# Kernel optimization log

Hardware: AMD Instinct MI355X
Metric: run time of the kernel (lower is better)

Reference implementation:

```python
import jax, jax.numpy as jnp
import numpy as np
from jax import lax

WINDOW_SIZE = 11
CHANNEL = 3
SIGMA = 1.5


def _build_window():
    # 1D gaussian, normalized, then outer product -> (C, 1, k, k) depthwise kernel
    coords = jnp.arange(WINDOW_SIZE, dtype=jnp.float32) - WINDOW_SIZE // 2
    g = jnp.exp(-coords ** 2 / (2.0 * SIGMA ** 2))
    g = g / g.sum()
    w2d = jnp.outer(g, g)  # (k, k)
    return jnp.broadcast_to(w2d[None, None], (CHANNEL, 1, WINDOW_SIZE, WINDOW_SIZE))


def _dwconv(x, w):
    pad = WINDOW_SIZE // 2
    return lax.conv_general_dilated(
        x, w,
        window_strides=(1, 1),
        padding=[(pad, pad), (pad, pad)],
        dimension_numbers=("NCHW", "OIHW", "NCHW"),
        feature_group_count=CHANNEL,
    )


def setup_inputs() -> dict:
    key = jax.random.key(0)
    k1, k2 = jax.random.split(key)
    pred = jax.random.uniform(k1, (16, 3, 512, 512), dtype=jnp.float32)
    target = jax.random.uniform(k2, (16, 3, 512, 512), dtype=jnp.float32)
    return {"pred": pred, "target": target}


def reference(pred, target):
    C1, C2 = 0.01 ** 2, 0.03 ** 2
    w = _build_window().astype(pred.dtype)

    mu_x = _dwconv(pred, w)
    mu_y = _dwconv(target, w)
    mu_x_sq = mu_x * mu_x
    mu_y_sq = mu_y * mu_y
    mu_xy = mu_x * mu_y

    sg_x = _dwconv(pred * pred, w) - mu_x_sq
    sg_y = _dwconv(target * target, w) - mu_y_sq
    sg_xy = _dwconv(pred * target, w) - mu_xy

    ssim_map = ((2.0 * mu_xy + C1) * (2.0 * sg_xy + C2)) / (
        (mu_x_sq + mu_y_sq + C1) * (sg_x + sg_y + C2)
    )
    return 1.0 - ssim_map.mean()
```

## Files before the change

kernel.cpp:

```cpp
#include <hip/hip_runtime.h>


namespace {
constexpr int IMG   = 512;
constexpr int NCH   = 48;
constexpr int TW    = 16;
constexpr int TH    = 64;
constexpr int RSTR  = 88;
constexpr int NSTR  = (TH + 16) / 16;
constexpr int TPX   = IMG / TW;
constexpr int TPY   = IMG / TH;
constexpr int NBLK  = TPX * TPY * NCH;

constexpr float Wf[11] = {
    0.00102838f, 0.00759876f, 0.03600077f, 0.10936069f, 0.21300554f,
    0.26601172f,
    0.21300554f, 0.10936069f, 0.03600077f, 0.00759876f, 0.00102838f };

constexpr float band_wc(int d) {
    return (d >= 0 && d < 11) ? Wf[d] : 0.f;
}

constexpr unsigned short f2h(float f) {
    if (f == 0.f) return 0;
    unsigned u = __builtin_bit_cast(unsigned, f);
    int  he = int((u >> 23) & 0xff) - 127 + 15;
    unsigned hm   = (u & 0x7fffff) >> 13;
    unsigned rest = u & 0x1fff;
    if (rest > 0x1000 || (rest == 0x1000 && (hm & 1))) ++hm;
    return (unsigned short)((unsigned(he) << 10) + hm);
}

struct Tabs { unsigned short a[64][8]; unsigned short b[64][8]; };
constexpr Tabs build_tabs() {
    Tabs t{};
    for (int lane = 0; lane < 64; ++lane) {
        const int nr = lane & 15, quad = lane >> 4;
        for (int jj = 0; jj < 8; ++jj) {
            const int k = quad * 8 + jj;
            t.a[lane][jj] = f2h(band_wc(k - nr));
            t.b[lane][jj] = f2h(band_wc(k - nr - 3));
        }
    }
    return t;
}
}

__device__ __constant__ __align__(16) Tabs g_tabs = build_tabs();

typedef _Float16 half8 __attribute__((ext_vector_type(8)));
typedef _Float16 half4v __attribute__((ext_vector_type(4)));
typedef _Float16 h2 __attribute__((ext_vector_type(2)));
typedef float float4v __attribute__((ext_vector_type(4)));
typedef float float2v __attribute__((ext_vector_type(2)));

__device__ inline h2 pk(float a, float b) {
    auto v = __builtin_amdgcn_cvt_pkrtz(a, b);
    h2 r;
    __builtin_memcpy(&r, &v, sizeof(r));
    return r;
}

union H8 { half8 v; h2 p[4]; };

__global__ __launch_bounds__(256, 8) void ssim_tile_kernel(
    const float* __restrict__ pred, const float* __restrict__ tgt,
    float* __restrict__ partial)
{
    __shared__ __align__(16) _Float16 hf_t[5][TW][RSTR];
    __shared__ float wred[4];

    const int t    = threadIdx.x;
    const int w    = t >> 6;
    const int lane = t & 63;
    const int nr   = lane & 15;
    const int quad = lane >> 4;

    const int bid  = blockIdx.x;
    const int img  = bid >> 8;
    const int tile = bid & 255;
    const int txi  = tile >> 3;
    const int tyi  = tile & 7;
    const int tx   = txi * TW;
    const int ty   = tyi * TH;

    const float* __restrict__ p = pred + (size_t)img * (IMG * IMG);
    const float* __restrict__ q = tgt  + (size_t)img * (IMG * IMG);

    const half8 Aband = *(const half8*)(g_tabs.a[lane]);
    const half8 Bband = *(const half8*)(g_tabs.b[lane]);
    const float4v zf = {0.f, 0.f, 0.f, 0.f};
    const half8 z8 = {};

    const int cb  = tx - 8 + (quad << 3);
    const int cbc = min(max(cb, 0), IMG - 8);
    const bool okc = ((unsigned)cb <= (unsigned)(IMG - 8));

    auto ld_stripe = [&](int s, float4& xa, float4& xb, float4& ya, float4& yb) {
        const int gy  = ty + 16 * s + nr - 5;
        const int gyc = min(max(gy, 0), IMG - 1);
        const float* rp = p + gyc * IMG + cbc;
        const float* rq = q + gyc * IMG + cbc;
        xa = *(const float4*)rp;
        xb = *(const float4*)(rp + 4);
        ya = *(const float4*)rq;
        yb = *(const float4*)(rq + 4);
    };

    auto proc_stripe = [&](int s, float4 xa, float4 xb, float4 ya, float4 yb) {
        const int gy = ty + 16 * s + nr - 5;
        const bool ok = ((unsigned)gy < (unsigned)IMG) && okc;

        H8 ax, ay;
        ax.p[0] = pk(xa.x, xa.y); ax.p[1] = pk(xa.z, xa.w);
        ax.p[2] = pk(xb.x, xb.y); ax.p[3] = pk(xb.z, xb.w);
        ay.p[0] = pk(ya.x, ya.y); ay.p[1] = pk(ya.z, ya.w);
        ay.p[2] = pk(yb.x, yb.y); ay.p[3] = pk(yb.z, yb.w);
        if (!ok) { ax.v = z8; ay.v = z8; }

        half8 fx  = ax.v;
        half8 fy  = ay.v;
        half8 fxx = fx * fx;
        half8 fyy = fy * fy;
        half8 fxy = fx * fy;

        float4v D[5];
        D[0] = __builtin_amdgcn_mfma_f32_16x16x32_f16(fx,  Bband, zf, 0, 0, 0);
        D[1] = __builtin_amdgcn_mfma_f32_16x16x32_f16(fy,  Bband, zf, 0, 0, 0);
        D[2] = __builtin_amdgcn_mfma_f32_16x16x32_f16(fxx, Bband, zf, 0, 0, 0);
        D[3] = __builtin_amdgcn_mfma_f32_16x16x32_f16(fyy, Bband, zf, 0, 0, 0);
        D[4] = __builtin_amdgcn_mfma_f32_16x16x32_f16(fxy, Bband, zf, 0, 0, 0);

        const int r0 = 16 * s + (quad << 2);
        #pragma unroll
        for (int f = 0; f < 5; ++f) {
            h2 lo = pk(D[f][0], D[f][1]);
            h2 hi = pk(D[f][2], D[f][3]);
            half4v hh = {lo[0], lo[1], hi[0], hi[1]};
            *(half4v*)&hf_t[f][nr][r0] = hh;
        }
    };

    {
        float4 xa0, xb0, ya0, yb0;
        ld_stripe(w, xa0, xb0, ya0, yb0);
        if (w == 0) {
            float4 xa1, xb1, ya1, yb1;
            ld_stripe(4, xa1, xb1, ya1, yb1);
            proc_stripe(0, xa0, xb0, ya0, yb0);
            proc_stripe(4, xa1, xb1, ya1, yb1);
        } else {
            proc_stripe(w, xa0, xb0, ya0, yb0);
        }
    }
    __syncthreads();

    constexpr float C1 = 1e-4f, C2 = 9e-4f;
    const float2v C1v = {C1, C1};
    const float2v C2v = {C2, C2};
    const float2v K12 = {C1 + C2, C1 + C2};
    float2v lsum2 = {0.f, 0.f};
    {
        const int rb = 16 * w + (quad << 3);
        float4v acc[5];
        #pragma unroll
        for (int f = 0; f < 5; ++f) {
            half8 bf = *(const half8*)&hf_t[f][nr][rb];
            acc[f] = __builtin_amdgcn_mfma_f32_16x16x32_f16(Aband, bf, zf, 0, 0, 0);
        }
        #pragma unroll
        for (int h = 0; h < 2; ++h) {
            float2v mx  = {acc[0][2*h], acc[0][2*h+1]};
            float2v my  = {acc[1][2*h], acc[1][2*h+1]};
            float2v ex2 = {acc[2][2*h], acc[2][2*h+1]};
            float2v ey2 = {acc[3][2*h], acc[3][2*h+1]};
            float2v exy = {acc[4][2*h], acc[4][2*h+1]};
            float2v P  = mx * my;
            float2v U  = mx * mx + my * my + C1v;
            float2v n1 = 2.f * P + C1v;
            float2v n2 = 2.f * (exy - P) + C2v;
            float2v num = n1 * n2;
            float2v e1 = (ex2 + ey2) - U + K12;
            float2v den = U * e1;
            float2v r = {__builtin_amdgcn_rcpf(den.x),
                         __builtin_amdgcn_rcpf(den.y)};
            lsum2 += num * r;
        }
    }
    float lsum = lsum2.x + lsum2.y;

    #pragma unroll
    for (int off = 32; off > 0; off >>= 1)
        lsum += __shfl_down(lsum, off, 64);
    if (lane == 0) wred[w] = lsum;
    __syncthreads();
    if (t == 0) partial[bid] = wred[0] + wred[1] + wred[2] + wred[3];
}

__global__ __launch_bounds__(1024) void ssim_finish(
    const float* __restrict__ partial, float* __restrict__ out)
{
    __shared__ float wred[16];
    const int t = threadIdx.x;
    float s = 0.f;
    #pragma unroll
    for (int i = 0; i < NBLK / 1024; ++i)
        s += partial[t + i * 1024];
    #pragma unroll
    for (int off = 32; off > 0; off >>= 1)
        s += __shfl_down(s, off, 64);
    if ((t & 63) == 0) wred[t >> 6] = s;
    __syncthreads();
    if (t == 0) {
        float acc = 0.f;
        #pragma unroll
        for (int i = 0; i < 16; ++i) acc += wred[i];
        out[0] = 1.f - acc * (1.f / (float)((long long)NCH * IMG * IMG));
    }
}

extern "C" void kernel_launch(void* const* d_in, const int* in_sizes, int n_in,
                              void* d_out, int out_size, void* d_ws, size_t ws_size,
                              hipStream_t stream)
{
    const float* pred = (const float*)d_in[0];
    const float* tgt  = (const float*)d_in[1];
    float* out     = (float*)d_out;
    float* partial = (float*)d_ws;

    ssim_tile_kernel<<<NBLK, 256, 0, stream>>>(pred, tgt, partial);
    ssim_finish<<<1, 1024, 0, stream>>>(partial, out);
}
```

Measured before the change: 139.1 us.

## Give each wave an independent 16x16 tile and drop block-level barriers

Restructures the SSIM kernel so each wavefront computes a full 16x16 output tile on its own, loading its 32-row halo and doing both horizontal and vertical band MFMAs through a per-wave LDS slot. This removes __syncthreads and the uneven stripe split in which one wave handled two stripes. In exchange, input halo reads and horizontal MFMA work per output double, and per-tile partial sums grow fourfold for the finish kernel. LDS use per field is reduced by reusing two slots sequentially.

```diff
diff --git a/kernel.cpp b/kernel.cpp
--- a/kernel.cpp
+++ b/kernel.cpp
@@ -4,13 +4,10 @@
 namespace {
 constexpr int IMG   = 512;
 constexpr int NCH   = 48;
-constexpr int TW    = 16;
-constexpr int TH    = 64;
-constexpr int RSTR  = 88;
-constexpr int NSTR  = (TH + 16) / 16;
-constexpr int TPX   = IMG / TW;
-constexpr int TPY   = IMG / TH;
-constexpr int NBLK  = TPX * TPY * NCH;
+constexpr int TPX   = IMG / 16;
+constexpr int NTILE = TPX * TPX * NCH;
+constexpr int NBLK  = NTILE / 4;
+constexpr int RS    = 40;
 
 constexpr float Wf[11] = {
     0.00102838f, 0.00759876f, 0.03600077f, 0.10936069f, 0.21300554f,
@@ -63,12 +60,11 @@
 
 union H8 { half8 v; h2 p[4]; };
 
-__global__ __launch_bounds__(256, 8) void ssim_tile_kernel(
+__global__ __launch_bounds__(256, 6) void ssim_fused_kernel(
     const float* __restrict__ pred, const float* __restrict__ tgt,
     float* __restrict__ partial)
 {
-    __shared__ __align__(16) _Float16 hf_t[5][TW][RSTR];
-    __shared__ float wred[4];
+    __shared__ __align__(16) _Float16 hf[4][2][16][RS];
 
     const int t    = threadIdx.x;
     const int w    = t >> 6;
@@ -76,13 +72,11 @@
     const int nr   = lane & 15;
     const int quad = lane >> 4;
 
-    const int bid  = blockIdx.x;
-    const int img  = bid >> 8;
-    const int tile = bid & 255;
-    const int txi  = tile >> 3;
-    const int tyi  = tile & 7;
-    const int tx   = txi * TW;
-    const int ty   = tyi * TH;
+    const int tid  = blockIdx.x * 4 + w;
+    const int img  = tid >> 10;
+    const int tile = tid & 1023;
+    const int tx   = (tile & 31) * 16;
+    const int ty   = (tile >> 5) * 16;
 
     const float* __restrict__ p = pred + (size_t)img * (IMG * IMG);
     const float* __restrict__ q = tgt  + (size_t)img * (IMG * IMG);
@@ -96,105 +90,92 @@
     const int cbc = min(max(cb, 0), IMG - 8);
     const bool okc = ((unsigned)cb <= (unsigned)(IMG - 8));
 
-    auto ld_stripe = [&](int s, float4& xa, float4& xb, float4& ya, float4& yb) {
+    float4 xa[2], xb[2], ya[2], yb[2];
+    bool ok[2];
+    #pragma unroll
+    for (int s = 0; s < 2; ++s) {
         const int gy  = ty + 16 * s + nr - 5;
         const int gyc = min(max(gy, 0), IMG - 1);
+        ok[s] = ((unsigned)gy < (unsigned)IMG) && okc;
         const float* rp = p + gyc * IMG + cbc;
         const float* rq = q + gyc * IMG + cbc;
-        xa = *(const float4*)rp;
-        xb = *(const float4*)(rp + 4);
-        ya = *(const float4*)rq;
-        yb = *(const float4*)(rq + 4);
-    };
-
-    auto proc_stripe = [&](int s, float4 xa, float4 xb, float4 ya, float4 yb) {
-        const int gy = ty + 16 * s + nr - 5;
-        const bool ok = ((unsigned)gy < (unsigned)IMG) && okc;
-
+        xa[s] = *(const float4*)rp;
+        xb[s] = *(const float4*)(rp + 4);
+        ya[s] = *(const float4*)rq;
+        yb[s] = *(const float4*)(rq + 4);
+    }
+
+    half8 fx[2], fy[2];
+    #pragma unroll
+    for (int s = 0; s < 2; ++s) {
         H8 ax, ay;
-        ax.p[0] = pk(xa.x, xa.y); ax.p[1] = pk(xa.z, xa.w);
-        ax.p[2] = pk(xb.x, xb.y); ax.p[3] = pk(xb.z, xb.w);
-        ay.p[0] = pk(ya.x, ya.y); ay.p[1] = pk(ya.z, ya.w);
-        ay.p[2] = pk(yb.x, yb.y); ay.p[3] = pk(yb.z, yb.w);
-        if (!ok) { ax.v = z8; ay.v = z8; }
-
-        half8 fx  = ax.v;
-        half8 fy  = ay.v;
-        half8 fxx = fx * fx;
-        half8 fyy = fy * fy;
-        half8 fxy = fx * fy;
-
-        float4v D[5];
-        D[0] = __builtin_amdgcn_mfma_f32_16x16x32_f16(fx,  Bband, zf, 0, 0, 0);
-        D[1] = __builtin_amdgcn_mfma_f32_16x16x32_f16(fy,  Bband, zf, 0, 0, 0);
-        D[2] = __builtin_amdgcn_mfma_f32_16x16x32_f16(fxx, Bband, zf, 0, 0, 0);
-        D[3] = __builtin_amdgcn_mfma_f32_16x16x32_f16(fyy, Bband, zf, 0, 0, 0);
-        D[4] = __builtin_amdgcn_mfma_f32_16x16x32_f16(fxy, Bband, zf, 0, 0, 0);
-
-        const int r0 = 16 * s + (quad << 2);
-        #pragma unroll
-        for (int f = 0; f < 5; ++f) {
-            h2 lo = pk(D[f][0], D[f][1]);
-            h2 hi = pk(D[f][2], D[f][3]);
-            half4v hh = {lo[0], lo[1], hi[0], hi[1]};
-            *(half4v*)&hf_t[f][nr][r0] = hh;
-        }
-    };
-
-    {
-        float4 xa0, xb0, ya0, yb0;
-        ld_stripe(w, xa0, xb0, ya0, yb0);
-        if (w == 0) {
-            float4 xa1, xb1, ya1, yb1;
-            ld_stripe(4, xa1, xb1, ya1, yb1);
-            proc_stripe(0, xa0, xb0, ya0, yb0);
-            proc_stripe(4, xa1, xb1, ya1, yb1);
-        } else {
-            proc_stripe(w, xa0, xb0, ya0, yb0);
-        }
-    }
-    __syncthreads();
+        ax.p[0] = pk(xa[s].x, xa[s].y); ax.p[1] = pk(xa[s].z, xa[s].w);
+        ax.p[2] = pk(xb[s].x, xb[s].y); ax.p[3] = pk(xb[s].z, xb[s].w);
+        ay.p[0] = pk(ya[s].x, ya[s].y); ay.p[1] = pk(ya[s].z, ya[s].w);
+        ay.p[2] = pk(yb[s].x, yb[s].y); ay.p[3] = pk(yb[s].z, yb[s].w);
+        if (!ok[s]) { ax.v = z8; ay.v = z8; }
+        fx[s] = ax.v;
+        fy[s] = ay.v;
+    }
+
+    const int wr = quad << 2;
+    auto hwrite = [&](int slot, int s, float4v d) {
+        h2 lo = pk(d[0], d[1]);
+        h2 hi = pk(d[2], d[3]);
+        half4v hh = {lo[0], lo[1], hi[0], hi[1]};
+        *(half4v*)&hf[w][slot][nr][16 * s + wr] = hh;
+    };
+    auto hread = [&](int slot) -> half8 {
+        return *(const half8*)&hf[w][slot][nr][quad << 3];
+    };
+    auto HM = [&](half8 a) {
+        return __builtin_amdgcn_mfma_f32_16x16x32_f16(a, Bband, zf, 0, 0, 0);
+    };
+    auto VM = [&](half8 b) {
+        return __builtin_amdgcn_mfma_f32_16x16x32_f16(Aband, b, zf, 0, 0, 0);
+    };
+
+    float4v acc[5];
+    hwrite(0, 0, HM(fx[0]));  hwrite(0, 1, HM(fx[1]));
+    hwrite(1, 0, HM(fy[0]));  hwrite(1, 1, HM(fy[1]));
+    acc[0] = VM(hread(0));
+    acc[1] = VM(hread(1));
+    hwrite(0, 0, HM(fx[0] * fx[0]));  hwrite(0, 1, HM(fx[1] * fx[1]));
+    hwrite(1, 0, HM(fy[0] * fy[0]));  hwrite(1, 1, HM(fy[1] * fy[1]));
+    acc[2] = VM(hread(0));
+    acc[3] = VM(hread(1));
+    hwrite(0, 0, HM(fx[0] * fy[0]));  hwrite(0, 1, HM(fx[1] * fy[1]));
+    acc[4] = VM(hread(0));
 
     constexpr float C1 = 1e-4f, C2 = 9e-4f;
     const float2v C1v = {C1, C1};
     const float2v C2v = {C2, C2};
     const float2v K12 = {C1 + C2, C1 + C2};
     float2v lsum2 = {0.f, 0.f};
-    {
-        const int rb = 16 * w + (quad << 3);
-        float4v acc[5];
-        #pragma unroll
-        for (int f = 0; f < 5; ++f) {
-            half8 bf = *(const half8*)&hf_t[f][nr][rb];
-            acc[f] = __builtin_amdgcn_mfma_f32_16x16x32_f16(Aband, bf, zf, 0, 0, 0);
-        }
-        #pragma unroll
-        for (int h = 0; h < 2; ++h) {
-            float2v mx  = {acc[0][2*h], acc[0][2*h+1]};
-            float2v my  = {acc[1][2*h], acc[1][2*h+1]};
-            float2v ex2 = {acc[2][2*h], acc[2][2*h+1]};
-            float2v ey2 = {acc[3][2*h], acc[3][2*h+1]};
-            float2v exy = {acc[4][2*h], acc[4][2*h+1]};
-            float2v P  = mx * my;
-            float2v U  = mx * mx + my * my + C1v;
-            float2v n1 = 2.f * P + C1v;
-            float2v n2 = 2.f * (exy - P) + C2v;
-            float2v num = n1 * n2;
-            float2v e1 = (ex2 + ey2) - U + K12;
-            float2v den = U * e1;
-            float2v r = {__builtin_amdgcn_rcpf(den.x),
-                         __builtin_amdgcn_rcpf(den.y)};
-            lsum2 += num * r;
-        }
+    #pragma unroll
+    for (int h = 0; h < 2; ++h) {
+        float2v mx  = {acc[0][2*h], acc[0][2*h+1]};
+        float2v my  = {acc[1][2*h], acc[1][2*h+1]};
+        float2v ex2 = {acc[2][2*h], acc[2][2*h+1]};
+        float2v ey2 = {acc[3][2*h], acc[3][2*h+1]};
+        float2v exy = {acc[4][2*h], acc[4][2*h+1]};
+        float2v P  = mx * my;
+        float2v U  = mx * mx + my * my + C1v;
+        float2v n1 = 2.f * P + C1v;
+        float2v n2 = 2.f * (exy - P) + C2v;
+        float2v num = n1 * n2;
+        float2v e1 = (ex2 + ey2) - U + K12;
+        float2v den = U * e1;
+        float2v r = {__builtin_amdgcn_rcpf(den.x),
+                     __builtin_amdgcn_rcpf(den.y)};
+        lsum2 += num * r;
     }
     float lsum = lsum2.x + lsum2.y;
 
     #pragma unroll
     for (int off = 32; off > 0; off >>= 1)
         lsum += __shfl_down(lsum, off, 64);
-    if (lane == 0) wred[w] = lsum;
-    __syncthreads();
-    if (t == 0) partial[bid] = wred[0] + wred[1] + wred[2] + wred[3];
+    if (lane == 0) partial[tid] = lsum;
 }
 
 __global__ __launch_bounds__(1024) void ssim_finish(
@@ -204,7 +185,7 @@
     const int t = threadIdx.x;
     float s = 0.f;
     #pragma unroll
-    for (int i = 0; i < NBLK / 1024; ++i)
+    for (int i = 0; i < NTILE / 1024; ++i)
         s += partial[t + i * 1024];
     #pragma unroll
     for (int off = 32; off > 0; off >>= 1)
@@ -228,6 +209,6 @@
     float* out     = (float*)d_out;
     float* partial = (float*)d_ws;
 
-    ssim_tile_kernel<<<NBLK, 256, 0, stream>>>(pred, tgt, partial);
+    ssim_fused_kernel<<<NBLK, 256, 0, stream>>>(pred, tgt, partial);
     ssim_finish<<<1, 1024, 0, stream>>>(partial, out);
 }
```

New measurement: 146.7 us. 1.05x slower.
